# Kernel optimization log

Hardware: AMD Instinct MI355X
Metric: run time of the kernel (lower is better)

Reference implementation:

```python
import jax, jax.numpy as jnp
import numpy as np

B, S, MODEL_DIM = 4, 512, 128
FEAT = 2 * MODEL_DIM  # hidden feature dim must be 2*model_dim for Ws


def setup_inputs() -> dict:
    key = jax.random.key(0)
    k1, k2, k3 = jax.random.split(key, 3)
    hidden = jax.random.normal(k1, (B, S, FEAT), dtype=jnp.float32)
    # nn.Linear(2*model_dim, model_dim, bias=False): weight [model_dim, 2*model_dim]
    Ws = jax.random.normal(k2, (MODEL_DIM, FEAT), dtype=jnp.float32) * (1.0 / np.sqrt(FEAT))
    # nn.Linear(model_dim, 1, bias=False): weight [1, model_dim]
    vs = jax.random.normal(k3, (1, MODEL_DIM), dtype=jnp.float32) * (1.0 / np.sqrt(MODEL_DIM))
    return {"hidden": hidden, "Ws": Ws, "vs": vs}


def reference(hidden, Ws, vs):
    # query*key broadcast: [B, S, S, 2D]
    prod = hidden[:, None, :, :] * hidden[:, :, None, :]
    # MLP score: Linear -> tanh -> Linear, squeeze -> [B, S, S]
    h = jnp.tanh(jnp.einsum('bqkf,df->bqkd', prod, Ws))
    sjt = jnp.einsum('bqkd,d->bqk', h, vs[0])
    atten = jax.nn.softmax(sjt, axis=2)  # dropout = identity (eval)
    context = jnp.einsum('bqk,bkf->bqf', atten, hidden)
    return (context, atten)
```

## Files before the change

### kernel.cpp

```cpp
#include <hip/hip_runtime.h>
#include <hip/hip_bf16.h>

#define Bb 4
#define Ss 512
#define Ff 256
#define Dd 128

typedef __attribute__((ext_vector_type(8))) short bf8_t;
typedef __attribute__((ext_vector_type(4))) float f32x4;

__device__ __forceinline__ short bfbits(float x) {
  union { __hip_bfloat16 b; short s; } u;
  u.b = __hip_bfloat16(x);
  return u.s;
}

__device__ __forceinline__ float fast_tanh(float x) {
  float e = exp2f(x * 2.8853900818f);
  return 1.0f - 2.0f * __builtin_amdgcn_rcpf(e + 1.0f);
}

typedef __attribute__((address_space(3))) unsigned int lds_u32;
typedef const __attribute__((address_space(1))) unsigned int glb_u32;
__device__ __forceinline__ void load_lds16(const void* g, void* l) {
  __builtin_amdgcn_global_load_lds((glb_u32*)g, (lds_u32*)l, 16, 0, 0);
}

__global__ __launch_bounds__(256) void cvt_kernel(const float* __restrict__ hidden,
                                                  short* __restrict__ hbf) {
  const int idx = blockIdx.x * 256 + threadIdx.x;
  const int lin = idx * 4;
  const float4 v = *(const float4*)(hidden + lin);
  const int r = lin >> 8;
  const int c = lin & 255;
  const int cs = c ^ ((r & 7) << 3);
  short4 o = make_short4(bfbits(v.x), bfbits(v.y), bfbits(v.z), bfbits(v.w));
  *(short4*)(hbf + ((size_t)r << 8) + cs) = o;
}

__global__ __launch_bounds__(256) void score_kernel(
    const float* __restrict__ hidden, const short* __restrict__ hbf,
    const float* __restrict__ Ws, const float* __restrict__ vs,
    float* __restrict__ Sws)
{
  __shared__ __align__(16) short htile[2][64 * 256];
  __shared__ float s_part[4][2][64];

  const int tid   = threadIdx.x;
  const int lane  = tid & 63;
  const int w     = tid >> 6;
  const int col16 = lane & 15;
  const int grp   = lane >> 4;

  const int blk  = blockIdx.x;
  const int pair = blk >> 2;
  const int b    = blk & 3;
  const int q0   = pair * 2;
  const int c0   = q0 >> 6;

  const float* Hb  = hidden + (size_t)b * Ss * Ff;
  const short* hsb = hbf + (size_t)b * Ss * Ff;
  float*       Sb  = Sws + (size_t)b * Ss * Ss;

  bf8_t afr[2][2][8];
  #pragma unroll
  for (int ks = 0; ks < 8; ++ks) {
    const int f0 = ks * 32 + grp * 8;
    float4 h0[2], h1[2];
    #pragma unroll
    for (int g = 0; g < 2; ++g) {
      const float* hq = Hb + (size_t)(q0 + g) * Ff + f0;
      h0[g] = *(const float4*)(hq);
      h1[g] = *(const float4*)(hq + 4);
    }
    #pragma unroll
    for (int mf = 0; mf < 2; ++mf) {
      const int d = w * 32 + mf * 16 + col16;
      const float* wr = Ws + (size_t)d * Ff + f0;
      const float4 w0 = *(const float4*)(wr);
      const float4 w1 = *(const float4*)(wr + 4);
      #pragma unroll
      for (int g = 0; g < 2; ++g) {
        bf8_t t;
        t[0] = bfbits(h0[g].x * w0.x); t[1] = bfbits(h0[g].y * w0.y);
        t[2] = bfbits(h0[g].z * w0.z); t[3] = bfbits(h0[g].w * w0.w);
        t[4] = bfbits(h1[g].x * w1.x); t[5] = bfbits(h1[g].y * w1.y);
        t[6] = bfbits(h1[g].z * w1.z); t[7] = bfbits(h1[g].w * w1.w);
        afr[g][mf][ks] = t;
      }
    }
  }

  float vsv[2][4];
  #pragma unroll
  for (int mf = 0; mf < 2; ++mf)
    #pragma unroll
    for (int r = 0; r < 4; ++r)
      vsv[mf][r] = vs[w * 32 + mf * 16 + grp * 4 + r];

  {
    const short* src = hsb + c0 * (64 * 256);
    #pragma unroll
    for (int i = 0; i < 8; ++i) {
      const int seg = i * 4 + w;
      load_lds16(src + seg * 512 + lane * 8, &htile[0][seg * 512]);
    }
  }

  const int swz = (col16 & 7) << 3;

  int cur = 0;
  for (int c = c0; c < 8; ++c) {
    const int k0 = c << 6;
    __syncthreads();
    if (c < 7) {
      const short* src = hsb + (c + 1) * (64 * 256);
      const int nb = cur ^ 1;
      #pragma unroll
      for (int i = 0; i < 8; ++i) {
        const int seg = i * 4 + w;
        load_lds16(src + seg * 512 + lane * 8, &htile[nb][seg * 512]);
      }
    }
    #pragma unroll
    for (int nf = 0; nf < 4; ++nf) {
      f32x4 acc[2][2] = {};
      const int rbase = nf * 4096 + col16 * 256;
      #pragma unroll
      for (int ks = 0; ks < 8; ++ks) {
        const int coff = (ks * 32 + grp * 8) ^ swz;
        const bf8_t bbv = *(const bf8_t*)(&htile[cur][rbase + coff]);
        acc[0][0] = __builtin_amdgcn_mfma_f32_16x16x32_bf16(afr[0][0][ks], bbv, acc[0][0], 0, 0, 0);
        acc[0][1] = __builtin_amdgcn_mfma_f32_16x16x32_bf16(afr[0][1][ks], bbv, acc[0][1], 0, 0, 0);
        acc[1][0] = __builtin_amdgcn_mfma_f32_16x16x32_bf16(afr[1][0][ks], bbv, acc[1][0], 0, 0, 0);
        acc[1][1] = __builtin_amdgcn_mfma_f32_16x16x32_bf16(afr[1][1][ks], bbv, acc[1][1], 0, 0, 0);
      }
      #pragma unroll
      for (int g = 0; g < 2; ++g) {
        float ps = 0.f;
        #pragma unroll
        for (int mf = 0; mf < 2; ++mf)
          #pragma unroll
          for (int r = 0; r < 4; ++r)
            ps += vsv[mf][r] * fast_tanh(acc[g][mf][r]);
        ps += __shfl_xor(ps, 16);
        ps += __shfl_xor(ps, 32);
        if (lane < 16) s_part[w][g][nf * 16 + lane] = ps;
      }
    }
    asm volatile("s_waitcnt lgkmcnt(0)" ::: "memory");
    __builtin_amdgcn_sched_barrier(0);
    __builtin_amdgcn_s_barrier();
    __builtin_amdgcn_sched_barrier(0);
    if (tid < 128) {
      const int g = tid >> 6, key = tid & 63;
      const int k = k0 + key;
      if (k >= q0) {
        const float v = s_part[0][g][key] + s_part[1][g][key] +
                        s_part[2][g][key] + s_part[3][g][key];
        Sb[(size_t)(q0 + g) * Ss + k] = v;
        if (k >= q0 + 2) Sb[(size_t)k * Ss + (q0 + g)] = v;
      }
    }
    cur ^= 1;
  }
}

__global__ __launch_bounds__(256) void ctx_kernel(
    const float* __restrict__ hidden, const float* __restrict__ Sws,
    float* __restrict__ out)
{
  __shared__ float p[4][512];
  __shared__ float ctxp[4][4][256];
  __shared__ float red[8];

  const int tid = threadIdx.x, lane = tid & 63, w = tid >> 6;
  const int blk = blockIdx.x;
  const int b   = blk >> 7;
  const int q0  = (blk & 127) * 4;

  const float* Sb = Sws + (size_t)b * Ss * Ss;
  const float* Hb = hidden + (size_t)b * Ss * Ff;
  float* att = out + (size_t)Bb * Ss * Ff + ((size_t)(b * Ss + q0)) * Ss;

  #pragma unroll
  for (int g = 0; g < 4; ++g) {
    const float s0 = Sb[(size_t)(q0 + g) * Ss + tid];
    const float s1 = Sb[(size_t)(q0 + g) * Ss + tid + 256];
    float m = fmaxf(s0, s1);
    #pragma unroll
    for (int d = 1; d < 64; d <<= 1) m = fmaxf(m, __shfl_xor(m, d));
    if (lane == 0) red[w] = m;
    __syncthreads();
    m = fmaxf(fmaxf(red[0], red[1]), fmaxf(red[2], red[3]));
    const float p0 = exp2f((s0 - m) * 1.44269504f);
    const float p1 = exp2f((s1 - m) * 1.44269504f);
    float sm = p0 + p1;
    #pragma unroll
    for (int d = 1; d < 64; d <<= 1) sm += __shfl_xor(sm, d);
    if (lane == 0) red[4 + w] = sm;
    __syncthreads();
    const float inv = 1.0f / (red[4] + red[5] + red[6] + red[7]);
    const float a0 = p0 * inv, a1 = p1 * inv;
    att[(size_t)g * Ss + tid]       = a0;
    att[(size_t)g * Ss + tid + 256] = a1;
    p[g][tid] = a0; p[g][tid + 256] = a1;
  }
  __syncthreads();

  float4 cg[4] = {{0,0,0,0},{0,0,0,0},{0,0,0,0},{0,0,0,0}};
  const float* hp = Hb + (size_t)(w * 128) * Ff + lane * 4;
  #pragma unroll 4
  for (int k = 0; k < 128; ++k) {
    const float4 h = *(const float4*)(hp + (size_t)k * Ff);
    #pragma unroll
    for (int g = 0; g < 4; ++g) {
      const float a = p[g][w * 128 + k];
      cg[g].x += a * h.x; cg[g].y += a * h.y; cg[g].z += a * h.z; cg[g].w += a * h.w;
    }
  }
  #pragma unroll
  for (int g = 0; g < 4; ++g)
    *(float4*)(&ctxp[w][g][lane * 4]) = cg[g];
  __syncthreads();
  #pragma unroll
  for (int rep = 0; rep < 4; ++rep) {
    const int idx = rep * 256 + tid;
    const int g = idx >> 8, f = idx & 255;
    out[((size_t)(b * Ss) + q0 + g) * Ff + f] =
        ctxp[0][g][f] + ctxp[1][g][f] + ctxp[2][g][f] + ctxp[3][g][f];
  }
}

__global__ __launch_bounds__(256) void selfatten_fallback(
    const float* __restrict__ hidden, const float* __restrict__ Ws,
    const float* __restrict__ vs, float* __restrict__ out)
{
  __shared__ __align__(16) short htile[2][64][264];
  __shared__ float s_part[2][4][2][64];
  __shared__ float s_full[2][512];
  __shared__ float red[8];

  const int tid = threadIdx.x, lane = tid & 63, w = tid >> 6;
  const int col16 = lane & 15, grp = lane >> 4;
  const int blk = blockIdx.x, b = blk >> 8, q0 = (blk & 255) * 2;
  const float* Hb = hidden + (size_t)b * Ss * Ff;

  bf8_t afr[2][2][8];
  #pragma unroll
  for (int ks = 0; ks < 8; ++ks) {
    const int f0 = ks * 32 + grp * 8;
    #pragma unroll
    for (int mf = 0; mf < 2; ++mf) {
      const int d = w * 32 + mf * 16 + col16;
      const float* wr = Ws + (size_t)d * Ff + f0;
      const float4 w0 = *(const float4*)(wr);
      const float4 w1 = *(const float4*)(wr + 4);
      #pragma unroll
      for (int g = 0; g < 2; ++g) {
        const float* hq = Hb + (size_t)(q0 + g) * Ff + f0;
        const float4 h0 = *(const float4*)(hq);
        const float4 h1 = *(const float4*)(hq + 4);
        bf8_t t;
        t[0] = bfbits(h0.x * w0.x); t[1] = bfbits(h0.y * w0.y);
        t[2] = bfbits(h0.z * w0.z); t[3] = bfbits(h0.w * w0.w);
        t[4] = bfbits(h1.x * w1.x); t[5] = bfbits(h1.y * w1.y);
        t[6] = bfbits(h1.z * w1.z); t[7] = bfbits(h1.w * w1.w);
        afr[g][mf][ks] = t;
      }
    }
  }
  float vsv[2][4];
  #pragma unroll
  for (int mf = 0; mf < 2; ++mf)
    #pragma unroll
    for (int r = 0; r < 4; ++r) vsv[mf][r] = vs[w * 32 + mf * 16 + grp * 4 + r];

  #pragma unroll
  for (int it = 0; it < 8; ++it) {
    const int lin = it * 2048 + tid * 8;
    const float4 v0 = *(const float4*)(Hb + lin);
    const float4 v1 = *(const float4*)(Hb + lin + 4);
    const int row = lin >> 8, col = lin & 255;
    bf8_t o;
    o[0] = bfbits(v0.x); o[1] = bfbits(v0.y); o[2] = bfbits(v0.z); o[3] = bfbits(v0.w);
    o[4] = bfbits(v1.x); o[5] = bfbits(v1.y); o[6] = bfbits(v1.z); o[7] = bfbits(v1.w);
    *(bf8_t*)(&htile[0][row][col]) = o;
  }
  __syncthreads();
  int cur = 0;
  for (int c = 0; c < 8; ++c) {
    const int k0 = c * 64, nxt = cur ^ 1, cb = c & 1;
    const float* src = Hb + (size_t)(k0 + 64) * Ff;
    #pragma unroll
    for (int nf = 0; nf < 4; ++nf) {
      float4 sv[4];
      if (c < 7) {
        #pragma unroll
        for (int i = 0; i < 2; ++i) {
          const int lin = (nf * 2 + i) * 2048 + tid * 8;
          sv[2 * i] = *(const float4*)(src + lin);
          sv[2 * i + 1] = *(const float4*)(src + lin + 4);
        }
      }
      f32x4 acc[2][2] = {};
      #pragma unroll
      for (int ks = 0; ks < 8; ++ks) {
        const bf8_t bbv = *(const bf8_t*)(&htile[cur][nf * 16 + col16][ks * 32 + grp * 8]);
        #pragma unroll
        for (int g = 0; g < 2; ++g) {
          acc[g][0] = __builtin_amdgcn_mfma_f32_16x16x32_bf16(afr[g][0][ks], bbv, acc[g][0], 0, 0, 0);
          acc[g][1] = __builtin_amdgcn_mfma_f32_16x16x32_bf16(afr[g][1][ks], bbv, acc[g][1], 0, 0, 0);
        }
      }
      #pragma unroll
      for (int g = 0; g < 2; ++g) {
        float ps = 0.f;
        #pragma unroll
        for (int mf = 0; mf < 2; ++mf)
          #pragma unroll
          for (int r = 0; r < 4; ++r) ps += vsv[mf][r] * fast_tanh(acc[g][mf][r]);
        ps += __shfl_xor(ps, 16);
        ps += __shfl_xor(ps, 32);
        if (lane < 16) s_part[cb][w][g][nf * 16 + lane] = ps;
      }
      if (c < 7) {
        #pragma unroll
        for (int i = 0; i < 2; ++i) {
          const int lin = (nf * 2 + i) * 2048 + tid * 8;
          const int row = lin >> 8, col = lin & 255;
          const float4 a = sv[2 * i], bsv = sv[2 * i + 1];
          bf8_t o;
          o[0] = bfbits(a.x); o[1] = bfbits(a.y); o[2] = bfbits(a.z); o[3] = bfbits(a.w);
          o[4] = bfbits(bsv.x); o[5] = bfbits(bsv.y); o[6] = bfbits(bsv.z); o[7] = bfbits(bsv.w);
          *(bf8_t*)(&htile[nxt][row][col]) = o;
        }
      }
    }
    __syncthreads();
    if (tid < 128) {
      const int g = tid >> 6, key = tid & 63;
      s_full[g][k0 + key] = s_part[cb][0][g][key] + s_part[cb][1][g][key] +
                            s_part[cb][2][g][key] + s_part[cb][3][g][key];
    }
    cur = nxt;
  }
  __syncthreads();
  float av[2][2];
  #pragma unroll
  for (int g = 0; g < 2; ++g) {
    const float s0 = s_full[g][tid], s1 = s_full[g][tid + 256];
    float m = fmaxf(s0, s1);
    #pragma unroll
    for (int d = 1; d < 64; d <<= 1) m = fmaxf(m, __shfl_xor(m, d));
    if (lane == 0) red[w] = m;
    __syncthreads();
    m = fmaxf(fmaxf(red[0], red[1]), fmaxf(red[2], red[3]));
    const float p0 = exp2f((s0 - m) * 1.44269504f);
    const float p1 = exp2f((s1 - m) * 1.44269504f);
    float sm = p0 + p1;
    #pragma unroll
    for (int d = 1; d < 64; d <<= 1) sm += __shfl_xor(sm, d);
    if (lane == 0) red[4 + w] = sm;
    __syncthreads();
    const float inv = 1.0f / (red[4] + red[5] + red[6] + red[7]);
    av[g][0] = p0 * inv; av[g][1] = p1 * inv;
    float* attp = out + (size_t)Bb * Ss * Ff + ((size_t)(b * Ss + q0 + g)) * Ss;
    attp[tid] = av[g][0];
    attp[tid + 256] = av[g][1];
    __syncthreads();
  }
  s_full[0][tid] = av[0][0]; s_full[0][tid + 256] = av[0][1];
  s_full[1][tid] = av[1][0]; s_full[1][tid + 256] = av[1][1];
  __syncthreads();
  float* ctxp = (float*)htile;
  float4 c0v = {0,0,0,0}, c1v = {0,0,0,0};
  const float* hp = Hb + (size_t)(w * 128) * Ff + lane * 4;
  #pragma unroll 8
  for (int k = 0; k < 128; ++k) {
    const float4 h = *(const float4*)(hp + (size_t)k * Ff);
    const float a0 = s_full[0][w * 128 + k];
    const float a1 = s_full[1][w * 128 + k];
    c0v.x += a0 * h.x; c0v.y += a0 * h.y; c0v.z += a0 * h.z; c0v.w += a0 * h.w;
    c1v.x += a1 * h.x; c1v.y += a1 * h.y; c1v.z += a1 * h.z; c1v.w += a1 * h.w;
  }
  *(float4*)(&ctxp[(w * 2 + 0) * 256 + lane * 4]) = c0v;
  *(float4*)(&ctxp[(w * 2 + 1) * 256 + lane * 4]) = c1v;
  __syncthreads();
  #pragma unroll
  for (int rep = 0; rep < 2; ++rep) {
    const int idx = tid + rep * 256;
    const int g = idx >> 8, f = idx & 255;
    out[((size_t)(b * Ss) + q0 + g) * Ff + f] =
        ctxp[(0 * 2 + g) * 256 + f] + ctxp[(1 * 2 + g) * 256 + f] +
        ctxp[(2 * 2 + g) * 256 + f] + ctxp[(3 * 2 + g) * 256 + f];
  }
}

extern "C" void kernel_launch(void* const* d_in, const int* in_sizes, int n_in,
                              void* d_out, int out_size, void* d_ws, size_t ws_size,
                              hipStream_t stream) {
  (void)in_sizes; (void)n_in; (void)out_size;
  const float* hidden = (const float*)d_in[0];
  const float* Ws     = (const float*)d_in[1];
  const float* vs     = (const float*)d_in[2];
  float* out          = (float*)d_out;

  const size_t hbf_bytes = (size_t)Bb * Ss * Ff * sizeof(short);
  const size_t sws_bytes = (size_t)Bb * Ss * Ss * sizeof(float);
  if (ws_size >= hbf_bytes + sws_bytes) {
    short* hbf = (short*)d_ws;
    float* Sws = (float*)((char*)d_ws + hbf_bytes);
    cvt_kernel<<<dim3(Bb * Ss * Ff / 4 / 256), dim3(256), 0, stream>>>(hidden, hbf);
    score_kernel<<<dim3(Bb * Ss / 2), dim3(256), 0, stream>>>(hidden, hbf, Ws, vs, Sws);
    ctx_kernel<<<dim3(Bb * Ss / 4), dim3(256), 0, stream>>>(hidden, Sws, out);
  } else {
    selfatten_fallback<<<dim3(Bb * Ss / 2), dim3(256), 0, stream>>>(hidden, Ws, vs, out);
  }
}
```

Before: 85.12 us.

## Split score key range across two blocks; batch eight queries per ctx block

The score kernel now uses 32-key chunks and splits each query pair's remaining triangular key range between two blocks. This doubles the grid and balances work across blocks, at the cost of recomputing the A fragments twice per pair. The ctx kernel handles eight queries per block and batches the softmax reductions so it needs fewer barriers, reusing each hidden row load across more queries. The trade-off is higher register and LDS pressure in ctx and more prologue work overall in score.

```diff
diff --git a/kernel.cpp b/kernel.cpp
--- a/kernel.cpp
+++ b/kernel.cpp
@@ -43,8 +43,8 @@
     const float* __restrict__ Ws, const float* __restrict__ vs,
     float* __restrict__ Sws)
 {
-  __shared__ __align__(16) short htile[2][64 * 256];
-  __shared__ float s_part[4][2][64];
+  __shared__ __align__(16) short htile[2][32 * 256];
+  __shared__ float s_part[4][2][32];
 
   const int tid   = threadIdx.x;
   const int lane  = tid & 63;
@@ -53,10 +53,17 @@
   const int grp   = lane >> 4;
 
   const int blk  = blockIdx.x;
-  const int pair = blk >> 2;
   const int b    = blk & 3;
+  const int ph   = blk >> 2;
+  const int pair = ph >> 1;
+  const int half = ph & 1;
   const int q0   = pair * 2;
-  const int c0   = q0 >> 6;
+  const int c0   = q0 >> 5;
+  const int n    = 16 - c0;
+  const int nlo  = (n + 1) >> 1;
+  const int ca   = half ? (c0 + nlo) : c0;
+  const int cb   = half ? 16 : (c0 + nlo);
+  if (ca >= cb) return;
 
   const float* Hb  = hidden + (size_t)b * Ss * Ff;
   const short* hsb = hbf + (size_t)b * Ss * Ff;
@@ -99,9 +106,9 @@
       vsv[mf][r] = vs[w * 32 + mf * 16 + grp * 4 + r];
 
   {
-    const short* src = hsb + c0 * (64 * 256);
-    #pragma unroll
-    for (int i = 0; i < 8; ++i) {
+    const short* src = hsb + ca * (32 * 256);
+    #pragma unroll
+    for (int i = 0; i < 4; ++i) {
       const int seg = i * 4 + w;
       load_lds16(src + seg * 512 + lane * 8, &htile[0][seg * 512]);
     }
@@ -110,20 +117,20 @@
   const int swz = (col16 & 7) << 3;
 
   int cur = 0;
-  for (int c = c0; c < 8; ++c) {
-    const int k0 = c << 6;
+  for (int c = ca; c < cb; ++c) {
+    const int k0 = c << 5;
     __syncthreads();
-    if (c < 7) {
-      const short* src = hsb + (c + 1) * (64 * 256);
+    if (c + 1 < cb) {
+      const short* src = hsb + (c + 1) * (32 * 256);
       const int nb = cur ^ 1;
       #pragma unroll
-      for (int i = 0; i < 8; ++i) {
+      for (int i = 0; i < 4; ++i) {
         const int seg = i * 4 + w;
         load_lds16(src + seg * 512 + lane * 8, &htile[nb][seg * 512]);
       }
     }
     #pragma unroll
-    for (int nf = 0; nf < 4; ++nf) {
+    for (int nf = 0; nf < 2; ++nf) {
       f32x4 acc[2][2] = {};
       const int rbase = nf * 4096 + col16 * 256;
       #pragma unroll
@@ -152,8 +159,8 @@
     __builtin_amdgcn_sched_barrier(0);
     __builtin_amdgcn_s_barrier();
     __builtin_amdgcn_sched_barrier(0);
-    if (tid < 128) {
-      const int g = tid >> 6, key = tid & 63;
+    if (tid < 64) {
+      const int g = tid >> 5, key = tid & 31;
       const int k = k0 + key;
       if (k >= q0) {
         const float v = s_part[0][g][key] + s_part[1][g][key] +
@@ -170,61 +177,70 @@
     const float* __restrict__ hidden, const float* __restrict__ Sws,
     float* __restrict__ out)
 {
-  __shared__ float p[4][512];
-  __shared__ float ctxp[4][4][256];
-  __shared__ float red[8];
+  __shared__ float p8[8][512];
+  __shared__ float ctxp[4][8][256];
+  __shared__ float redm[8][4], reds[8][4];
 
   const int tid = threadIdx.x, lane = tid & 63, w = tid >> 6;
   const int blk = blockIdx.x;
-  const int b   = blk >> 7;
-  const int q0  = (blk & 127) * 4;
+  const int b   = blk >> 6;
+  const int q0  = (blk & 63) * 8;
 
   const float* Sb = Sws + (size_t)b * Ss * Ss;
   const float* Hb = hidden + (size_t)b * Ss * Ff;
   float* att = out + (size_t)Bb * Ss * Ff + ((size_t)(b * Ss + q0)) * Ss;
 
-  #pragma unroll
-  for (int g = 0; g < 4; ++g) {
-    const float s0 = Sb[(size_t)(q0 + g) * Ss + tid];
-    const float s1 = Sb[(size_t)(q0 + g) * Ss + tid + 256];
-    float m = fmaxf(s0, s1);
+  float s0[8], s1[8];
+  #pragma unroll
+  for (int g = 0; g < 8; ++g) {
+    s0[g] = Sb[(size_t)(q0 + g) * Ss + tid];
+    s1[g] = Sb[(size_t)(q0 + g) * Ss + tid + 256];
+    float m = fmaxf(s0[g], s1[g]);
     #pragma unroll
     for (int d = 1; d < 64; d <<= 1) m = fmaxf(m, __shfl_xor(m, d));
-    if (lane == 0) red[w] = m;
-    __syncthreads();
-    m = fmaxf(fmaxf(red[0], red[1]), fmaxf(red[2], red[3]));
-    const float p0 = exp2f((s0 - m) * 1.44269504f);
-    const float p1 = exp2f((s1 - m) * 1.44269504f);
+    if (lane == 0) redm[g][w] = m;
+  }
+  __syncthreads();
+  #pragma unroll
+  for (int g = 0; g < 8; ++g) {
+    const float m = fmaxf(fmaxf(redm[g][0], redm[g][1]), fmaxf(redm[g][2], redm[g][3]));
+    const float p0 = exp2f((s0[g] - m) * 1.44269504f);
+    const float p1 = exp2f((s1[g] - m) * 1.44269504f);
+    s0[g] = p0; s1[g] = p1;
     float sm = p0 + p1;
     #pragma unroll
     for (int d = 1; d < 64; d <<= 1) sm += __shfl_xor(sm, d);
-    if (lane == 0) red[4 + w] = sm;
-    __syncthreads();
-    const float inv = 1.0f / (red[4] + red[5] + red[6] + red[7]);
-    const float a0 = p0 * inv, a1 = p1 * inv;
+    if (lane == 0) reds[g][w] = sm;
+  }
+  __syncthreads();
+  #pragma unroll
+  for (int g = 0; g < 8; ++g) {
+    const float inv = 1.0f / (reds[g][0] + reds[g][1] + reds[g][2] + reds[g][3]);
+    const float a0 = s0[g] * inv, a1 = s1[g] * inv;
     att[(size_t)g * Ss + tid]       = a0;
     att[(size_t)g * Ss + tid + 256] = a1;
-    p[g][tid] = a0; p[g][tid + 256] = a1;
-  }
-  __syncthreads();
-
-  float4 cg[4] = {{0,0,0,0},{0,0,0,0},{0,0,0,0},{0,0,0,0}};
+    p8[g][tid] = a0; p8[g][tid + 256] = a1;
+  }
+  __syncthreads();
+
+  float4 cg[8] = {{0,0,0,0},{0,0,0,0},{0,0,0,0},{0,0,0,0},
+                  {0,0,0,0},{0,0,0,0},{0,0,0,0},{0,0,0,0}};
   const float* hp = Hb + (size_t)(w * 128) * Ff + lane * 4;
-  #pragma unroll 4
+  #pragma unroll 2
   for (int k = 0; k < 128; ++k) {
     const float4 h = *(const float4*)(hp + (size_t)k * Ff);
     #pragma unroll
-    for (int g = 0; g < 4; ++g) {
-      const float a = p[g][w * 128 + k];
+    for (int g = 0; g < 8; ++g) {
+      const float a = p8[g][w * 128 + k];
       cg[g].x += a * h.x; cg[g].y += a * h.y; cg[g].z += a * h.z; cg[g].w += a * h.w;
     }
   }
   #pragma unroll
-  for (int g = 0; g < 4; ++g)
+  for (int g = 0; g < 8; ++g)
     *(float4*)(&ctxp[w][g][lane * 4]) = cg[g];
   __syncthreads();
   #pragma unroll
-  for (int rep = 0; rep < 4; ++rep) {
+  for (int rep = 0; rep < 8; ++rep) {
     const int idx = rep * 256 + tid;
     const int g = idx >> 8, f = idx & 255;
     out[((size_t)(b * Ss) + q0 + g) * Ff + f] =
@@ -412,8 +428,8 @@
     short* hbf = (short*)d_ws;
     float* Sws = (float*)((char*)d_ws + hbf_bytes);
     cvt_kernel<<<dim3(Bb * Ss * Ff / 4 / 256), dim3(256), 0, stream>>>(hidden, hbf);
-    score_kernel<<<dim3(Bb * Ss / 2), dim3(256), 0, stream>>>(hidden, hbf, Ws, vs, Sws);
-    ctx_kernel<<<dim3(Bb * Ss / 4), dim3(256), 0, stream>>>(hidden, Sws, out);
+    score_kernel<<<dim3(Bb * Ss), dim3(256), 0, stream>>>(hidden, hbf, Ws, vs, Sws);
+    ctx_kernel<<<dim3(Bb * Ss / 8), dim3(256), 0, stream>>>(hidden, Sws, out);
   } else {
     selfatten_fallback<<<dim3(Bb * Ss / 2), dim3(256), 0, stream>>>(hidden, Ws, vs, out);
   }
```

Result: slower. 102.9 us (+20.9%).

## Use 32-key chunks with LDS atomic accumulation and per-wave softmax rows

Applied to the files above, without the earlier changes.

The score kernel now streams 32-key tiles instead of 64, which halves the LDS tile footprint. Per-chunk partial sums are accumulated with LDS atomicAdd into a full 512-entry score row, so the per-chunk barrier plus reduce-and-store step is gone and the global writes happen once at the end. The ctx kernel's softmax gives each wave its own query row with float4 loads and wave-only reductions, which removes the block-level barriers. The trade-offs are more chunk iterations, LDS atomic contention, and extra zero-initialization work.

```diff
diff --git a/kernel.cpp b/kernel.cpp
--- a/kernel.cpp
+++ b/kernel.cpp
@@ -43,8 +43,8 @@
     const float* __restrict__ Ws, const float* __restrict__ vs,
     float* __restrict__ Sws)
 {
-  __shared__ __align__(16) short htile[2][64 * 256];
-  __shared__ float s_part[4][2][64];
+  __shared__ __align__(16) short htile[2][32 * 256];
+  __shared__ float s_full[2][512];
 
   const int tid   = threadIdx.x;
   const int lane  = tid & 63;
@@ -53,10 +53,10 @@
   const int grp   = lane >> 4;
 
   const int blk  = blockIdx.x;
+  const int b    = blk & 3;
   const int pair = blk >> 2;
-  const int b    = blk & 3;
   const int q0   = pair * 2;
-  const int c0   = q0 >> 6;
+  const int c0   = q0 >> 5;
 
   const float* Hb  = hidden + (size_t)b * Ss * Ff;
   const short* hsb = hbf + (size_t)b * Ss * Ff;
@@ -99,9 +99,15 @@
       vsv[mf][r] = vs[w * 32 + mf * 16 + grp * 4 + r];
 
   {
-    const short* src = hsb + c0 * (64 * 256);
-    #pragma unroll
-    for (int i = 0; i < 8; ++i) {
+    float* sf = (float*)s_full;
+    #pragma unroll
+    for (int i = 0; i < 4; ++i) sf[i * 256 + tid] = 0.f;
+  }
+
+  {
+    const short* src = hsb + c0 * (32 * 256);
+    #pragma unroll
+    for (int i = 0; i < 4; ++i) {
       const int seg = i * 4 + w;
       load_lds16(src + seg * 512 + lane * 8, &htile[0][seg * 512]);
     }
@@ -110,20 +116,20 @@
   const int swz = (col16 & 7) << 3;
 
   int cur = 0;
-  for (int c = c0; c < 8; ++c) {
-    const int k0 = c << 6;
+  for (int c = c0; c < 16; ++c) {
+    const int k0 = c << 5;
     __syncthreads();
-    if (c < 7) {
-      const short* src = hsb + (c + 1) * (64 * 256);
+    if (c < 15) {
+      const short* src = hsb + (c + 1) * (32 * 256);
       const int nb = cur ^ 1;
       #pragma unroll
-      for (int i = 0; i < 8; ++i) {
+      for (int i = 0; i < 4; ++i) {
         const int seg = i * 4 + w;
         load_lds16(src + seg * 512 + lane * 8, &htile[nb][seg * 512]);
       }
     }
     #pragma unroll
-    for (int nf = 0; nf < 4; ++nf) {
+    for (int nf = 0; nf < 2; ++nf) {
       f32x4 acc[2][2] = {};
       const int rbase = nf * 4096 + col16 * 256;
       #pragma unroll
@@ -145,24 +151,20 @@
             ps += vsv[mf][r] * fast_tanh(acc[g][mf][r]);
         ps += __shfl_xor(ps, 16);
         ps += __shfl_xor(ps, 32);
-        if (lane < 16) s_part[w][g][nf * 16 + lane] = ps;
-      }
-    }
-    asm volatile("s_waitcnt lgkmcnt(0)" ::: "memory");
-    __builtin_amdgcn_sched_barrier(0);
-    __builtin_amdgcn_s_barrier();
-    __builtin_amdgcn_sched_barrier(0);
-    if (tid < 128) {
-      const int g = tid >> 6, key = tid & 63;
-      const int k = k0 + key;
-      if (k >= q0) {
-        const float v = s_part[0][g][key] + s_part[1][g][key] +
-                        s_part[2][g][key] + s_part[3][g][key];
-        Sb[(size_t)(q0 + g) * Ss + k] = v;
-        if (k >= q0 + 2) Sb[(size_t)k * Ss + (q0 + g)] = v;
+        if (lane < 16)
+          atomicAdd(&s_full[g][k0 + nf * 16 + lane], ps);
       }
     }
     cur ^= 1;
+  }
+  __syncthreads();
+
+  #pragma unroll
+  for (int g = 0; g < 2; ++g) {
+    for (int k = q0 + tid; k < Ss; k += 256)
+      Sb[(size_t)(q0 + g) * Ss + k] = s_full[g][k];
+    for (int k = q0 + 2 + tid; k < Ss; k += 256)
+      Sb[(size_t)k * Ss + (q0 + g)] = s_full[g][k];
   }
 }
 
@@ -172,7 +174,6 @@
 {
   __shared__ float p[4][512];
   __shared__ float ctxp[4][4][256];
-  __shared__ float red[8];
 
   const int tid = threadIdx.x, lane = tid & 63, w = tid >> 6;
   const int blk = blockIdx.x;
@@ -181,30 +182,32 @@
 
   const float* Sb = Sws + (size_t)b * Ss * Ss;
   const float* Hb = hidden + (size_t)b * Ss * Ff;
-  float* att = out + (size_t)Bb * Ss * Ff + ((size_t)(b * Ss + q0)) * Ss;
-
-  #pragma unroll
-  for (int g = 0; g < 4; ++g) {
-    const float s0 = Sb[(size_t)(q0 + g) * Ss + tid];
-    const float s1 = Sb[(size_t)(q0 + g) * Ss + tid + 256];
-    float m = fmaxf(s0, s1);
+
+  {
+    const int q = q0 + w;
+    const float* Srow = Sb + (size_t)q * Ss;
+    const float4 x0 = *(const float4*)(Srow + lane * 8);
+    const float4 x1 = *(const float4*)(Srow + lane * 8 + 4);
+    float m = fmaxf(fmaxf(fmaxf(x0.x, x0.y), fmaxf(x0.z, x0.w)),
+                    fmaxf(fmaxf(x1.x, x1.y), fmaxf(x1.z, x1.w)));
     #pragma unroll
     for (int d = 1; d < 64; d <<= 1) m = fmaxf(m, __shfl_xor(m, d));
-    if (lane == 0) red[w] = m;
-    __syncthreads();
-    m = fmaxf(fmaxf(red[0], red[1]), fmaxf(red[2], red[3]));
-    const float p0 = exp2f((s0 - m) * 1.44269504f);
-    const float p1 = exp2f((s1 - m) * 1.44269504f);
-    float sm = p0 + p1;
+    float4 e0, e1;
+    e0.x = exp2f((x0.x - m) * 1.44269504f); e0.y = exp2f((x0.y - m) * 1.44269504f);
+    e0.z = exp2f((x0.z - m) * 1.44269504f); e0.w = exp2f((x0.w - m) * 1.44269504f);
+    e1.x = exp2f((x1.x - m) * 1.44269504f); e1.y = exp2f((x1.y - m) * 1.44269504f);
+    e1.z = exp2f((x1.z - m) * 1.44269504f); e1.w = exp2f((x1.w - m) * 1.44269504f);
+    float sm = e0.x + e0.y + e0.z + e0.w + e1.x + e1.y + e1.z + e1.w;
     #pragma unroll
     for (int d = 1; d < 64; d <<= 1) sm += __shfl_xor(sm, d);
-    if (lane == 0) red[4 + w] = sm;
-    __syncthreads();
-    const float inv = 1.0f / (red[4] + red[5] + red[6] + red[7]);
-    const float a0 = p0 * inv, a1 = p1 * inv;
-    att[(size_t)g * Ss + tid]       = a0;
-    att[(size_t)g * Ss + tid + 256] = a1;
-    p[g][tid] = a0; p[g][tid + 256] = a1;
+    const float inv = 1.0f / sm;
+    e0.x *= inv; e0.y *= inv; e0.z *= inv; e0.w *= inv;
+    e1.x *= inv; e1.y *= inv; e1.z *= inv; e1.w *= inv;
+    float* att = out + (size_t)Bb * Ss * Ff + ((size_t)(b * Ss + q)) * Ss;
+    *(float4*)(att + lane * 8)     = e0;
+    *(float4*)(att + lane * 8 + 4) = e1;
+    *(float4*)(&p[w][lane * 8])     = e0;
+    *(float4*)(&p[w][lane * 8 + 4]) = e1;
   }
   __syncthreads();
 
```

Result: slower. 87.82 us (+3.2%).
